# Optimization experiments

Hardware: AMD Instinct MI355X
Metric: run time of the kernel (lower is better)

Reference implementation:

```python
import jax, jax.numpy as jnp
import numpy as np
from jax import lax

DIM = 128
N_CODEBOOKS = 8
CODEBOOK_SIZE = 2048
BATCH = 16
TOKENS = 2048


def setup_inputs() -> dict:
    key = jax.random.key(0)
    k1, k2 = jax.random.split(key)
    x = jax.random.normal(k1, (BATCH, DIM, TOKENS), dtype=jnp.float32)
    # matches nn.Parameter(torch.randn(K, D) / D**0.5) per stage, stacked
    codebooks = jax.random.normal(k2, (N_CODEBOOKS, CODEBOOK_SIZE, DIM),
                                  dtype=jnp.float32) / jnp.sqrt(jnp.float32(DIM))
    return {"x": x, "codebooks": codebooks}


def reference(x, codebooks):
    """Residual VQ forward.

    x: (B, D, T), codebooks: (n_cb, K, D)
    Returns (total_quantized (B,D,T), codes (B,n_cb,T) int32, commitment_loss scalar)
    """
    xt = jnp.transpose(x, (0, 2, 1))  # (B, T, D)

    def step(carry, cb):
        residual, total = carry  # (B,T,D) each; cb: (K,D)
        # squared euclidean distances: ||r||^2 - 2 r.c + ||c||^2 -> (B,T,K)
        dist = (jnp.sum(residual * residual, axis=-1, keepdims=True)
                - 2.0 * jnp.einsum('btd,kd->btk', residual, cb)
                + jnp.sum(cb * cb, axis=-1))
        idx = jnp.argmin(dist, axis=-1)          # (B, T)
        quantized = cb[idx]                       # gather -> (B, T, D)
        # straight-through combine
        q_st = residual + lax.stop_gradient(quantized - residual)
        total = total + q_st
        residual = residual - lax.stop_gradient(quantized)
        # F.mse_loss(residual.detach(), zeros) == mean(residual**2), detached
        loss = jnp.mean(lax.stop_gradient(residual) ** 2)
        return (residual, total), (idx.astype(jnp.int32), loss)

    init = (xt, jnp.zeros_like(xt))
    (_, total), (codes, losses) = lax.scan(step, init, codebooks)
    total_quantized = jnp.transpose(total, (0, 2, 1))   # (B, D, T)
    codes = jnp.transpose(codes, (1, 0, 2))             # (B, n_cb, T)
    commitment_loss = jnp.sum(losses)
    return total_quantized, codes, commitment_loss
```

## Files before the change

kernel.cpp:

```cpp
#include <hip/hip_runtime.h>

#define DIM 128
#define NCB 8
#define KSZ 2048
#define BATCH 16
#define TOK 2048
#define NTOK (BATCH * TOK)
#define NELEM (BATCH * DIM * TOK)
#define T_TILE 128
#define NTHR 512
#define CHUNK 64
#define NCHUNK (KSZ / CHUNK)

typedef float f32x4 __attribute__((ext_vector_type(4)));
typedef short s16x8 __attribute__((ext_vector_type(8)));

__device__ __forceinline__ unsigned short f2bf(float f) {
    unsigned u = __float_as_uint(f);
    u = (u + 0x7FFFu + ((u >> 16) & 1u)) >> 16;
    return (unsigned short)u;
}
__device__ __forceinline__ float bf2f(unsigned short h) {
    return __uint_as_float(((unsigned)h) << 16);
}

__global__ void rvq_prep_hi(const float* __restrict__ cbs,
                            unsigned short* __restrict__ ch) {
    int i = blockIdx.x * 256 + threadIdx.x;
    ch[i] = f2bf(cbs[i]);
}

__global__ void rvq_cnorm(const float* __restrict__ cbs,
                          float* __restrict__ cnorm,
                          float* __restrict__ loss_acc) {
    if (blockIdx.x == 0 && threadIdx.x == 0) *loss_acc = 0.0f;
    int k = blockIdx.x * 256 + threadIdx.x;
    const float4* row = (const float4*)(cbs + (size_t)k * DIM);
    float s = 0.0f;
#pragma unroll
    for (int i = 0; i < DIM / 4; ++i) {
        float4 v = row[i];
        s += v.x * v.x + v.y * v.y + v.z * v.z + v.w * v.w;
    }
    cnorm[k] = s;
}

__global__ __launch_bounds__(NTHR, 2) void rvq_fused(
        const float* __restrict__ x,
        const float* __restrict__ cbs,
        const unsigned short* __restrict__ ch,
        const float* __restrict__ cng,
        float* __restrict__ out,
        float* __restrict__ codes,
        float* __restrict__ loss_acc) {
    __shared__ float res_lds[T_TILE][DIM + 4];
    __shared__ unsigned short Bbuf[2][8192];
    __shared__ float mv1[T_TILE * 16];
    __shared__ int   mi1[T_TILE * 16];
    __shared__ float mv2[T_TILE * 16];
    __shared__ int   mi2[T_TILE * 16];
    __shared__ int   best4s[T_TILE][4];

    const int tid   = threadIdx.x;
    const int lane  = tid & 63;
    const int wv    = __builtin_amdgcn_readfirstlane(tid >> 6);
    const int col16 = lane & 15;
    const int quad  = lane >> 4;

    const int token0 = blockIdx.x * T_TILE;
    const int b      = token0 >> 11;
    const int t_in_b = token0 & (TOK - 1);

    {
        const float* xb = x + (size_t)b * DIM * TOK + t_in_b;
#pragma unroll
        for (int it = 0; it < 8; ++it) {
            int idx = it * NTHR + tid;
            int d  = idx >> 5;
            int t4 = (idx & 31) * 4;
            float4 v = *(const float4*)(xb + (size_t)d * TOK + t4);
            res_lds[t4 + 0][d] = v.x;
            res_lds[t4 + 1][d] = v.y;
            res_lds[t4 + 2][d] = v.z;
            res_lds[t4 + 3][d] = v.w;
        }
    }
    __syncthreads();

    float my_loss = 0.0f;

#define STAGE_PREFETCH(cc)                                                     \
    {                                                                          \
        int _f0 = wv * 2, _f1 = wv * 2 + 1;                                    \
        stg0 = *(const s16x8*)(ch_s +                                          \
            ((size_t)((cc) * CHUNK + (_f0 >> 2) * 16 + col16)) * DIM +         \
            ((_f0 & 3) * 32 + quad * 8));                                      \
        stg1 = *(const s16x8*)(ch_s +                                          \
            ((size_t)((cc) * CHUNK + (_f1 >> 2) * 16 + col16)) * DIM +         \
            ((_f1 & 3) * 32 + quad * 8));                                      \
    }

#define STAGE_WRITE(buf)                                                       \
    {                                                                          \
        *(s16x8*)&Bbuf[buf][(wv * 2) * 512 + lane * 8]     = stg0;             \
        *(s16x8*)&Bbuf[buf][(wv * 2 + 1) * 512 + lane * 8] = stg1;             \
    }

#define COMPUTE(accv, buf)                                                     \
    {                                                                          \
        _Pragma("unroll")                                                      \
        for (int nt = 0; nt < 4; ++nt) accv[nt] = (f32x4){0.f, 0.f, 0.f, 0.f}; \
        _Pragma("unroll")                                                      \
        for (int dc = 0; dc < 4; ++dc) {                                       \
            s16x8 bh0 = *(const s16x8*)&Bbuf[buf][(0 + dc) * 512 + lane * 8];  \
            s16x8 bh1 = *(const s16x8*)&Bbuf[buf][(4 + dc) * 512 + lane * 8];  \
            s16x8 bh2 = *(const s16x8*)&Bbuf[buf][(8 + dc) * 512 + lane * 8];  \
            s16x8 bh3 = *(const s16x8*)&Bbuf[buf][(12 + dc) * 512 + lane * 8]; \
            accv[0] = __builtin_amdgcn_mfma_f32_16x16x32_bf16(ah[dc], bh0, accv[0], 0, 0, 0); \
            accv[1] = __builtin_amdgcn_mfma_f32_16x16x32_bf16(ah[dc], bh1, accv[1], 0, 0, 0); \
            accv[2] = __builtin_amdgcn_mfma_f32_16x16x32_bf16(ah[dc], bh2, accv[2], 0, 0, 0); \
            accv[3] = __builtin_amdgcn_mfma_f32_16x16x32_bf16(ah[dc], bh3, accv[3], 0, 0, 0); \
            accv[0] = __builtin_amdgcn_mfma_f32_16x16x32_bf16(al[dc], bh0, accv[0], 0, 0, 0); \
            accv[1] = __builtin_amdgcn_mfma_f32_16x16x32_bf16(al[dc], bh1, accv[1], 0, 0, 0); \
            accv[2] = __builtin_amdgcn_mfma_f32_16x16x32_bf16(al[dc], bh2, accv[2], 0, 0, 0); \
            accv[3] = __builtin_amdgcn_mfma_f32_16x16x32_bf16(al[dc], bh3, accv[3], 0, 0, 0); \
        }                                                                      \
    }

#define FOLD(accv, cc)                                                         \
    {                                                                          \
        int _ib0 = (cc) * CHUNK + col16;                                       \
        float _cn0 = cn_s[_ib0], _cn1 = cn_s[_ib0 + 16];                       \
        float _cn2 = cn_s[_ib0 + 32], _cn3 = cn_s[_ib0 + 48];                  \
        _Pragma("unroll")                                                      \
        for (int r = 0; r < 4; ++r) {                                          \
            float p0 = fmaf(-2.0f, accv[0][r], _cn0);                          \
            float p1 = fmaf(-2.0f, accv[1][r], _cn1);                          \
            float p2 = fmaf(-2.0f, accv[2][r], _cn2);                          \
            float p3 = fmaf(-2.0f, accv[3][r], _cn3);                          \
            bool c01 = p1 < p0;                                                \
            float m01 = c01 ? p1 : p0; int j01 = c01 ? _ib0 + 16 : _ib0;       \
            bool c23 = p3 < p2;                                                \
            float m23 = c23 ? p3 : p2; int j23 = c23 ? _ib0 + 48 : _ib0 + 32;  \
            bool cf = m23 < m01;                                               \
            float m = cf ? m23 : m01; int jm = cf ? j23 : j01;                 \
            bool b1 = m < v1[r];                                               \
            bool b2 = m < v2[r];                                               \
            v2[r] = b1 ? v1[r] : (b2 ? m : v2[r]);                             \
            i2[r] = b1 ? i1[r] : (b2 ? jm : i2[r]);                            \
            v1[r] = b1 ? m : v1[r];                                            \
            i1[r] = b1 ? jm : i1[r];                                           \
        }                                                                      \
    }

#pragma unroll 1
    for (int s = 0; s < NCB; ++s) {
        const unsigned short* __restrict__ ch_s = ch  + (size_t)s * KSZ * DIM;
        const float* __restrict__ cb_s = cbs + (size_t)s * KSZ * DIM;
        const float* __restrict__ cn_s = cng + (size_t)s * KSZ;

        s16x8 ah[4], al[4];
#pragma unroll
        for (int dc = 0; dc < 4; ++dc) {
            int t  = wv * 16 + col16;
            int d0 = dc * 32 + quad * 8;
            float4 u = *(const float4*)&res_lds[t][d0];
            float4 w = *(const float4*)&res_lds[t][d0 + 4];
            float e[8] = {u.x, u.y, u.z, u.w, w.x, w.y, w.z, w.w};
            s16x8 hv, lv;
#pragma unroll
            for (int j = 0; j < 8; ++j) {
                unsigned short h = f2bf(e[j]);
                hv[j] = (short)h;
                lv[j] = (short)f2bf(e[j] - bf2f(h));
            }
            ah[dc] = hv;
            al[dc] = lv;
        }

        float v1[4], v2[4]; int i1[4], i2[4];
#pragma unroll
        for (int r = 0; r < 4; ++r) {
            v1[r] = 3.4e38f; v2[r] = 3.4e38f; i1[r] = 0; i2[r] = 0;
        }

        s16x8 stg0, stg1;
        f32x4 accA[4], accB[4];

        STAGE_PREFETCH(0); STAGE_WRITE(0); __syncthreads();
        STAGE_PREFETCH(1);
        COMPUTE(accA, 0);
        STAGE_WRITE(1); __syncthreads();
#pragma unroll 1
        for (int c = 1; c < 31; c += 2) {
            STAGE_PREFETCH(c + 1);
            COMPUTE(accB, 1);
            FOLD(accA, c - 1);
            STAGE_WRITE(0);
            __syncthreads();
            STAGE_PREFETCH(c + 2);
            COMPUTE(accA, 0);
            FOLD(accB, c);
            STAGE_WRITE(1);
            __syncthreads();
        }
        COMPUTE(accB, 1);
        FOLD(accA, 30);
        FOLD(accB, 31);

#pragma unroll
        for (int r = 0; r < 4; ++r) {
            int t = wv * 16 + quad * 4 + r;
            mv1[t * 16 + col16] = v1[r];
            mi1[t * 16 + col16] = i1[r];
            mv2[t * 16 + col16] = v2[r];
            mi2[t * 16 + col16] = i2[r];
        }
        __syncthreads();

        if (tid < T_TILE) {
            const int t = tid;
            float bv[4] = {3.4e38f, 3.4e38f, 3.4e38f, 3.4e38f};
            int   bi[4] = {0x7FFFFFFF, 0x7FFFFFFF, 0x7FFFFFFF, 0x7FFFFFFF};
#pragma unroll
            for (int col = 0; col < 16; ++col) {
#pragma unroll
                for (int w = 0; w < 2; ++w) {
                    float v = w ? mv2[t * 16 + col] : mv1[t * 16 + col];
                    int   i = w ? mi2[t * 16 + col] : mi1[t * 16 + col];
#pragma unroll
                    for (int j = 0; j < 4; ++j) {
                        if (v < bv[j] || (v == bv[j] && i < bi[j])) {
                            float tv = bv[j]; bv[j] = v; v = tv;
                            int   ti = bi[j]; bi[j] = i; i = ti;
                        }
                    }
                }
            }
#pragma unroll
            for (int j = 0; j < 4; ++j) best4s[t][j] = bi[j];
        }
        __syncthreads();

        {
            const int t  = tid >> 2;
            const int cs = tid & 3;
            const int cand = best4s[t][cs];
            const float* crow = cb_s + (size_t)cand * DIM;
            float n0 = 0, n1 = 0, n2 = 0, n3 = 0;
            float a0 = 0, a1 = 0, a2 = 0, a3 = 0;
#pragma unroll 8
            for (int d4 = 0; d4 < DIM / 4; ++d4) {
                float4 r4 = *(const float4*)&res_lds[t][d4 * 4];
                float4 q4 = *(const float4*)&crow[d4 * 4];
                n0 = fmaf(r4.x, r4.x, n0); n1 = fmaf(r4.y, r4.y, n1);
                n2 = fmaf(r4.z, r4.z, n2); n3 = fmaf(r4.w, r4.w, n3);
                a0 = fmaf(r4.x, q4.x, a0); a1 = fmaf(r4.y, q4.y, a1);
                a2 = fmaf(r4.z, q4.z, a2); a3 = fmaf(r4.w, q4.w, a3);
            }
            float rn  = (n0 + n1) + (n2 + n3);
            float dot = (a0 + a1) + (a2 + a3);
            float dist = fmaf(-2.0f, dot, rn) + cn_s[cand];
            int best = cand;
#pragma unroll
            for (int mk = 1; mk <= 2; mk <<= 1) {
                float od = __shfl_xor(dist, mk, 64);
                int   oi = __shfl_xor(best, mk, 64);
                if (od < dist || (od == dist && oi < best)) {
                    dist = od; best = oi;
                }
            }
            if (cs == 0)
                codes[(size_t)b * (NCB * TOK) + (size_t)s * TOK + t_in_b + t] =
                    (float)best;
            const float* qrow = cb_s + (size_t)best * DIM;
            float lp = 0.0f;
#pragma unroll
            for (int d4 = 0; d4 < 8; ++d4) {
                int d = cs * 32 + d4 * 4;
                float4 r4 = *(const float4*)&res_lds[t][d];
                float4 q4 = *(const float4*)&qrow[d];
                float4 nr;
                nr.x = r4.x - q4.x; nr.y = r4.y - q4.y;
                nr.z = r4.z - q4.z; nr.w = r4.w - q4.w;
                *(float4*)&res_lds[t][d] = nr;
                lp += nr.x * nr.x + nr.y * nr.y + nr.z * nr.z + nr.w * nr.w;
            }
            my_loss += lp;
        }
        __syncthreads();
    }

    {
        const float* xb = x + (size_t)b * DIM * TOK + t_in_b;
        float* ob = out + (size_t)b * DIM * TOK + t_in_b;
#pragma unroll
        for (int it = 0; it < 8; ++it) {
            int idx = it * NTHR + tid;
            int d  = idx >> 5;
            int t4 = (idx & 31) * 4;
            float4 v = *(const float4*)(xb + (size_t)d * TOK + t4);
            float4 o;
            o.x = v.x - res_lds[t4 + 0][d];
            o.y = v.y - res_lds[t4 + 1][d];
            o.z = v.z - res_lds[t4 + 2][d];
            o.w = v.w - res_lds[t4 + 3][d];
            *(float4*)(ob + (size_t)d * TOK + t4) = o;
        }
    }

#pragma unroll
    for (int off = 32; off > 0; off >>= 1)
        my_loss += __shfl_down(my_loss, off, 64);
    if (lane == 0) atomicAdd(loss_acc, my_loss);
}

__global__ void rvq_loss_fin(const float* __restrict__ loss_acc,
                             float* __restrict__ loss_out) {
    *loss_out = *loss_acc * (1.0f / (float)NELEM);
}

extern "C" void kernel_launch(void* const* d_in, const int* in_sizes, int n_in,
                              void* d_out, int out_size, void* d_ws, size_t ws_size,
                              hipStream_t stream) {
    const float* x   = (const float*)d_in[0];
    const float* cbs = (const float*)d_in[1];

    float* out      = (float*)d_out;
    float* codes    = out + NELEM;
    float* loss_out = out + NELEM + (size_t)BATCH * NCB * TOK;

    float* wsf      = (float*)d_ws;
    float* loss_acc = wsf;
    unsigned short* ch = (unsigned short*)(wsf + 256);
    float* cng = (float*)(ch + (size_t)NCB * KSZ * DIM);

    hipLaunchKernelGGL(rvq_prep_hi, dim3((NCB * KSZ * DIM) / 256), dim3(256),
                       0, stream, cbs, ch);
    hipLaunchKernelGGL(rvq_cnorm, dim3((NCB * KSZ) / 256), dim3(256), 0, stream,
                       cbs, cng, loss_acc);
    hipLaunchKernelGGL(rvq_fused, dim3(NTOK / T_TILE), dim3(NTHR), 0, stream,
                       x, cbs, ch, cng, out, codes, loss_acc);
    hipLaunchKernelGGL(rvq_loss_fin, dim3(1), dim3(1), 0, stream,
                       loss_acc, loss_out);
}
```

Measured before the change: 548.6 us.

## Switch RVQ distance GEMM to single-pass fp16 MFMA with grouped top-2 candidates

Drops the bf16 hi/lo split, which needed two MFMA passes, in favour of a single fp16 MFMA pass, halving the matrix work per codebook. Work is reorganised so each pair of waves owns a 512-code group and covers 64 tokens × 32 codes per chunk, reusing A fragments across four M-tiles. Chunk IDs are packed into the low mantissa bits so the running top-2 is kept with plain fminf/fmaxf instead of index tracking. Per-group top-2 values then feed an exact fp32 rescoring of four candidates per group. This risks wrong argmin choices from the fp16 rounding and the mantissa-bit packing, and raises register pressure from the 16-slot state and ah[4][4].

Result: slower. 603.6 us (+10.0%).

```diff
diff --git a/kernel.cpp b/kernel.cpp
--- a/kernel.cpp
+++ b/kernel.cpp
@@ -9,25 +9,17 @@
 #define NELEM (BATCH * DIM * TOK)
 #define T_TILE 128
 #define NTHR 512
-#define CHUNK 64
-#define NCHUNK (KSZ / CHUNK)
+#define CHUNK 32
+#define NCHUNK 16
+#define GCODES 512
 
 typedef float f32x4 __attribute__((ext_vector_type(4)));
-typedef short s16x8 __attribute__((ext_vector_type(8)));
-
-__device__ __forceinline__ unsigned short f2bf(float f) {
-    unsigned u = __float_as_uint(f);
-    u = (u + 0x7FFFu + ((u >> 16) & 1u)) >> 16;
-    return (unsigned short)u;
-}
-__device__ __forceinline__ float bf2f(unsigned short h) {
-    return __uint_as_float(((unsigned)h) << 16);
-}
-
-__global__ void rvq_prep_hi(const float* __restrict__ cbs,
-                            unsigned short* __restrict__ ch) {
+typedef _Float16 f16x8 __attribute__((ext_vector_type(8)));
+
+__global__ void rvq_prep_f16(const float* __restrict__ cbs,
+                             _Float16* __restrict__ chf) {
     int i = blockIdx.x * 256 + threadIdx.x;
-    ch[i] = f2bf(cbs[i]);
+    chf[i] = (_Float16)cbs[i];
 }
 
 __global__ void rvq_cnorm(const float* __restrict__ cbs,
@@ -48,24 +40,25 @@
 __global__ __launch_bounds__(NTHR, 2) void rvq_fused(
         const float* __restrict__ x,
         const float* __restrict__ cbs,
-        const unsigned short* __restrict__ ch,
+        const _Float16* __restrict__ chf,
         const float* __restrict__ cng,
         float* __restrict__ out,
         float* __restrict__ codes,
         float* __restrict__ loss_acc) {
     __shared__ float res_lds[T_TILE][DIM + 4];
-    __shared__ unsigned short Bbuf[2][8192];
-    __shared__ float mv1[T_TILE * 16];
-    __shared__ int   mi1[T_TILE * 16];
-    __shared__ float mv2[T_TILE * 16];
-    __shared__ int   mi2[T_TILE * 16];
-    __shared__ int   best4s[T_TILE][4];
+    __shared__ __align__(16) char shbuf[T_TILE * 144 * 4];
+    __shared__ float cn_lds[KSZ];
+
+    _Float16* Ball = (_Float16*)shbuf;
+    float*    cand = (float*)shbuf;
 
     const int tid   = threadIdx.x;
     const int lane  = tid & 63;
     const int wv    = __builtin_amdgcn_readfirstlane(tid >> 6);
     const int col16 = lane & 15;
     const int quad  = lane >> 4;
+    const int g     = wv >> 1;
+    const int sub   = wv & 1;
 
     const int token0 = blockIdx.x * T_TILE;
     const int b      = token0 >> 11;
@@ -88,198 +81,228 @@
     __syncthreads();
 
     float my_loss = 0.0f;
-
-#define STAGE_PREFETCH(cc)                                                     \
-    {                                                                          \
-        int _f0 = wv * 2, _f1 = wv * 2 + 1;                                    \
-        stg0 = *(const s16x8*)(ch_s +                                          \
-            ((size_t)((cc) * CHUNK + (_f0 >> 2) * 16 + col16)) * DIM +         \
-            ((_f0 & 3) * 32 + quad * 8));                                      \
-        stg1 = *(const s16x8*)(ch_s +                                          \
-            ((size_t)((cc) * CHUNK + (_f1 >> 2) * 16 + col16)) * DIM +         \
-            ((_f1 & 3) * 32 + quad * 8));                                      \
-    }
-
-#define STAGE_WRITE(buf)                                                       \
-    {                                                                          \
-        *(s16x8*)&Bbuf[buf][(wv * 2) * 512 + lane * 8]     = stg0;             \
-        *(s16x8*)&Bbuf[buf][(wv * 2 + 1) * 512 + lane * 8] = stg1;             \
-    }
-
-#define COMPUTE(accv, buf)                                                     \
-    {                                                                          \
-        _Pragma("unroll")                                                      \
-        for (int nt = 0; nt < 4; ++nt) accv[nt] = (f32x4){0.f, 0.f, 0.f, 0.f}; \
-        _Pragma("unroll")                                                      \
-        for (int dc = 0; dc < 4; ++dc) {                                       \
-            s16x8 bh0 = *(const s16x8*)&Bbuf[buf][(0 + dc) * 512 + lane * 8];  \
-            s16x8 bh1 = *(const s16x8*)&Bbuf[buf][(4 + dc) * 512 + lane * 8];  \
-            s16x8 bh2 = *(const s16x8*)&Bbuf[buf][(8 + dc) * 512 + lane * 8];  \
-            s16x8 bh3 = *(const s16x8*)&Bbuf[buf][(12 + dc) * 512 + lane * 8]; \
-            accv[0] = __builtin_amdgcn_mfma_f32_16x16x32_bf16(ah[dc], bh0, accv[0], 0, 0, 0); \
-            accv[1] = __builtin_amdgcn_mfma_f32_16x16x32_bf16(ah[dc], bh1, accv[1], 0, 0, 0); \
-            accv[2] = __builtin_amdgcn_mfma_f32_16x16x32_bf16(ah[dc], bh2, accv[2], 0, 0, 0); \
-            accv[3] = __builtin_amdgcn_mfma_f32_16x16x32_bf16(ah[dc], bh3, accv[3], 0, 0, 0); \
-            accv[0] = __builtin_amdgcn_mfma_f32_16x16x32_bf16(al[dc], bh0, accv[0], 0, 0, 0); \
-            accv[1] = __builtin_amdgcn_mfma_f32_16x16x32_bf16(al[dc], bh1, accv[1], 0, 0, 0); \
-            accv[2] = __builtin_amdgcn_mfma_f32_16x16x32_bf16(al[dc], bh2, accv[2], 0, 0, 0); \
-            accv[3] = __builtin_amdgcn_mfma_f32_16x16x32_bf16(al[dc], bh3, accv[3], 0, 0, 0); \
-        }                                                                      \
-    }
-
-#define FOLD(accv, cc)                                                         \
-    {                                                                          \
-        int _ib0 = (cc) * CHUNK + col16;                                       \
-        float _cn0 = cn_s[_ib0], _cn1 = cn_s[_ib0 + 16];                       \
-        float _cn2 = cn_s[_ib0 + 32], _cn3 = cn_s[_ib0 + 48];                  \
-        _Pragma("unroll")                                                      \
-        for (int r = 0; r < 4; ++r) {                                          \
-            float p0 = fmaf(-2.0f, accv[0][r], _cn0);                          \
-            float p1 = fmaf(-2.0f, accv[1][r], _cn1);                          \
-            float p2 = fmaf(-2.0f, accv[2][r], _cn2);                          \
-            float p3 = fmaf(-2.0f, accv[3][r], _cn3);                          \
-            bool c01 = p1 < p0;                                                \
-            float m01 = c01 ? p1 : p0; int j01 = c01 ? _ib0 + 16 : _ib0;       \
-            bool c23 = p3 < p2;                                                \
-            float m23 = c23 ? p3 : p2; int j23 = c23 ? _ib0 + 48 : _ib0 + 32;  \
-            bool cf = m23 < m01;                                               \
-            float m = cf ? m23 : m01; int jm = cf ? j23 : j01;                 \
-            bool b1 = m < v1[r];                                               \
-            bool b2 = m < v2[r];                                               \
-            v2[r] = b1 ? v1[r] : (b2 ? m : v2[r]);                             \
-            i2[r] = b1 ? i1[r] : (b2 ? jm : i2[r]);                            \
-            v1[r] = b1 ? m : v1[r];                                            \
-            i1[r] = b1 ? jm : i1[r];                                           \
-        }                                                                      \
-    }
+    const float INFV = __builtin_inff();
 
 #pragma unroll 1
     for (int s = 0; s < NCB; ++s) {
-        const unsigned short* __restrict__ ch_s = ch  + (size_t)s * KSZ * DIM;
+        const _Float16* __restrict__ ch_s = chf + (size_t)s * KSZ * DIM;
         const float* __restrict__ cb_s = cbs + (size_t)s * KSZ * DIM;
         const float* __restrict__ cn_s = cng + (size_t)s * KSZ;
 
-        s16x8 ah[4], al[4];
-#pragma unroll
-        for (int dc = 0; dc < 4; ++dc) {
-            int t  = wv * 16 + col16;
-            int d0 = dc * 32 + quad * 8;
-            float4 u = *(const float4*)&res_lds[t][d0];
-            float4 w = *(const float4*)&res_lds[t][d0 + 4];
-            float e[8] = {u.x, u.y, u.z, u.w, w.x, w.y, w.z, w.w};
-            s16x8 hv, lv;
-#pragma unroll
-            for (int j = 0; j < 8; ++j) {
-                unsigned short h = f2bf(e[j]);
-                hv[j] = (short)h;
-                lv[j] = (short)f2bf(e[j] - bf2f(h));
-            }
-            ah[dc] = hv;
-            al[dc] = lv;
-        }
-
-        float v1[4], v2[4]; int i1[4], i2[4];
-#pragma unroll
-        for (int r = 0; r < 4; ++r) {
-            v1[r] = 3.4e38f; v2[r] = 3.4e38f; i1[r] = 0; i2[r] = 0;
-        }
-
-        s16x8 stg0, stg1;
-        f32x4 accA[4], accB[4];
-
-        STAGE_PREFETCH(0); STAGE_WRITE(0); __syncthreads();
-        STAGE_PREFETCH(1);
-        COMPUTE(accA, 0);
-        STAGE_WRITE(1); __syncthreads();
+        {
+            float4 v = *(const float4*)(cn_s + tid * 4);
+            *(float4*)&cn_lds[tid * 4] = v;
+        }
+
+        f16x8 ah[4][4];
+#pragma unroll
+        for (int mt = 0; mt < 4; ++mt) {
+#pragma unroll
+            for (int dc = 0; dc < 4; ++dc) {
+                int t  = sub * 64 + mt * 16 + col16;
+                int d0 = dc * 32 + quad * 8;
+                float4 u = *(const float4*)&res_lds[t][d0];
+                float4 w = *(const float4*)&res_lds[t][d0 + 4];
+                f16x8 hv;
+                hv[0] = (_Float16)u.x; hv[1] = (_Float16)u.y;
+                hv[2] = (_Float16)u.z; hv[3] = (_Float16)u.w;
+                hv[4] = (_Float16)w.x; hv[5] = (_Float16)w.y;
+                hv[6] = (_Float16)w.z; hv[7] = (_Float16)w.w;
+                ah[mt][dc] = hv;
+            }
+        }
+
+        float k1[16], k2[16];
+#pragma unroll
+        for (int sl = 0; sl < 16; ++sl) { k1[sl] = INFV; k2[sl] = INFV; }
+
+        f16x8 stg[4];
+        _Float16* Bg = Ball + g * 2 * 4096;
+
+#pragma unroll
+        for (int j = 0; j < 4; ++j) {
+            int f = sub * 4 + j;
+            int nt = f >> 2, dc = f & 3;
+            stg[j] = *(const f16x8*)(ch_s +
+                (size_t)(g * GCODES + nt * 16 + col16) * DIM + dc * 32 + quad * 8);
+        }
+#pragma unroll
+        for (int j = 0; j < 4; ++j) {
+            int f = sub * 4 + j;
+            *(f16x8*)(Bg + f * 512 + lane * 8) = stg[j];
+        }
+        __syncthreads();
+
+        f32x4 acc[4][2];
 #pragma unroll 1
-        for (int c = 1; c < 31; c += 2) {
-            STAGE_PREFETCH(c + 1);
-            COMPUTE(accB, 1);
-            FOLD(accA, c - 1);
-            STAGE_WRITE(0);
+        for (int c = 0; c < NCHUNK; ++c) {
+            const int cur = c & 1;
+            if (c < NCHUNK - 1) {
+#pragma unroll
+                for (int j = 0; j < 4; ++j) {
+                    int f = sub * 4 + j;
+                    int nt = f >> 2, dc = f & 3;
+                    stg[j] = *(const f16x8*)(ch_s +
+                        (size_t)(g * GCODES + (c + 1) * CHUNK + nt * 16 + col16) * DIM
+                        + dc * 32 + quad * 8);
+                }
+            }
+#pragma unroll
+            for (int mt = 0; mt < 4; ++mt) {
+                acc[mt][0] = (f32x4){0.f, 0.f, 0.f, 0.f};
+                acc[mt][1] = (f32x4){0.f, 0.f, 0.f, 0.f};
+            }
+#pragma unroll
+            for (int dc = 0; dc < 4; ++dc) {
+                f16x8 b0 = *(const f16x8*)(Bg + cur * 4096 + dc * 512 + lane * 8);
+                f16x8 b1 = *(const f16x8*)(Bg + cur * 4096 + (4 + dc) * 512 + lane * 8);
+#pragma unroll
+                for (int mt = 0; mt < 4; ++mt) {
+                    acc[mt][0] = __builtin_amdgcn_mfma_f32_16x16x32_f16(
+                        ah[mt][dc], b0, acc[mt][0], 0, 0, 0);
+                    acc[mt][1] = __builtin_amdgcn_mfma_f32_16x16x32_f16(
+                        ah[mt][dc], b1, acc[mt][1], 0, 0, 0);
+                }
+            }
+            {
+                float cn0 = cn_lds[g * GCODES + c * CHUNK + col16];
+                float cn1 = cn_lds[g * GCODES + c * CHUNK + 16 + col16];
+                unsigned em = (unsigned)(c << 1);
+#pragma unroll
+                for (int mt = 0; mt < 4; ++mt) {
+#pragma unroll
+                    for (int r = 0; r < 4; ++r) {
+                        float p0 = fmaf(-2.0f, acc[mt][0][r], cn0);
+                        float p1 = fmaf(-2.0f, acc[mt][1][r], cn1);
+                        float q0 = __uint_as_float(
+                            (__float_as_uint(p0) & 0xFFFFFFE0u) | em);
+                        float q1 = __uint_as_float(
+                            (__float_as_uint(p1) & 0xFFFFFFE0u) | em | 1u);
+                        float m = fminf(q0, q1);
+                        int sl = mt * 4 + r;
+                        k2[sl] = fminf(k2[sl], fmaxf(k1[sl], m));
+                        k1[sl] = fminf(k1[sl], m);
+                    }
+                }
+            }
+            if (c < NCHUNK - 1) {
+#pragma unroll
+                for (int j = 0; j < 4; ++j) {
+                    int f = sub * 4 + j;
+                    *(f16x8*)(Bg + (cur ^ 1) * 4096 + f * 512 + lane * 8) = stg[j];
+                }
+            }
             __syncthreads();
-            STAGE_PREFETCH(c + 2);
-            COMPUTE(accA, 0);
-            FOLD(accB, c);
-            STAGE_WRITE(1);
-            __syncthreads();
-        }
-        COMPUTE(accB, 1);
-        FOLD(accA, 30);
-        FOLD(accB, 31);
-
-#pragma unroll
-        for (int r = 0; r < 4; ++r) {
-            int t = wv * 16 + quad * 4 + r;
-            mv1[t * 16 + col16] = v1[r];
-            mi1[t * 16 + col16] = i1[r];
-            mv2[t * 16 + col16] = v2[r];
-            mi2[t * 16 + col16] = i2[r];
-        }
-        __syncthreads();
-
-        if (tid < T_TILE) {
-            const int t = tid;
-            float bv[4] = {3.4e38f, 3.4e38f, 3.4e38f, 3.4e38f};
-            int   bi[4] = {0x7FFFFFFF, 0x7FFFFFFF, 0x7FFFFFFF, 0x7FFFFFFF};
-#pragma unroll
-            for (int col = 0; col < 16; ++col) {
-#pragma unroll
-                for (int w = 0; w < 2; ++w) {
-                    float v = w ? mv2[t * 16 + col] : mv1[t * 16 + col];
-                    int   i = w ? mi2[t * 16 + col] : mi1[t * 16 + col];
-#pragma unroll
-                    for (int j = 0; j < 4; ++j) {
-                        if (v < bv[j] || (v == bv[j] && i < bi[j])) {
-                            float tv = bv[j]; bv[j] = v; v = tv;
-                            int   ti = bi[j]; bi[j] = i; i = ti;
-                        }
-                    }
-                }
-            }
-#pragma unroll
-            for (int j = 0; j < 4; ++j) best4s[t][j] = bi[j];
+        }
+
+#pragma unroll
+        for (int mt = 0; mt < 4; ++mt) {
+#pragma unroll
+            for (int r = 0; r < 4; ++r) {
+                int t = sub * 64 + mt * 16 + quad * 4 + r;
+                int sl = mt * 4 + r;
+                float2 pr; pr.x = k1[sl]; pr.y = k2[sl];
+                *(float2*)&cand[t * 144 + g * 36 + col16 * 2] = pr;
+            }
         }
         __syncthreads();
 
         {
             const int t  = tid >> 2;
-            const int cs = tid & 3;
-            const int cand = best4s[t][cs];
-            const float* crow = cb_s + (size_t)cand * DIM;
+            const int gg = tid & 3;
+            float bk[4];
+            int   bcol[4];
+#pragma unroll
+            for (int jj = 0; jj < 4; ++jj) { bk[jj] = INFV; bcol[jj] = 0; }
+            const float* base = &cand[t * 144 + gg * 36];
+#pragma unroll
+            for (int j = 0; j < 8; ++j) {
+                float4 v4 = *(const float4*)(base + j * 4);
+                float vv[4] = {v4.x, v4.y, v4.z, v4.w};
+#pragma unroll
+                for (int e = 0; e < 4; ++e) {
+                    float v = vv[e];
+                    int col = (j * 4 + e) >> 1;
+#pragma unroll
+                    for (int jj = 0; jj < 4; ++jj) {
+                        bool lt = v < bk[jj];
+                        float tv = bk[jj]; int tc = bcol[jj];
+                        bk[jj] = lt ? v : bk[jj];
+                        bcol[jj] = lt ? col : bcol[jj];
+                        v = lt ? tv : v;
+                        col = lt ? tc : col;
+                    }
+                }
+            }
+            int cds[4];
+#pragma unroll
+            for (int jj = 0; jj < 4; ++jj) {
+                unsigned e = __float_as_uint(bk[jj]) & 0x1Fu;
+                cds[jj] = gg * GCODES + (int)((e >> 1) << 5) +
+                          (int)((e & 1) << 4) + bcol[jj];
+            }
+            const float* p0 = cb_s + (size_t)cds[0] * DIM;
+            const float* p1 = cb_s + (size_t)cds[1] * DIM;
+            const float* p2 = cb_s + (size_t)cds[2] * DIM;
+            const float* p3 = cb_s + (size_t)cds[3] * DIM;
             float n0 = 0, n1 = 0, n2 = 0, n3 = 0;
-            float a0 = 0, a1 = 0, a2 = 0, a3 = 0;
+            float a[4][4];
+#pragma unroll
+            for (int jj = 0; jj < 4; ++jj)
+#pragma unroll
+                for (int e = 0; e < 4; ++e) a[jj][e] = 0.0f;
 #pragma unroll 8
             for (int d4 = 0; d4 < DIM / 4; ++d4) {
                 float4 r4 = *(const float4*)&res_lds[t][d4 * 4];
-                float4 q4 = *(const float4*)&crow[d4 * 4];
                 n0 = fmaf(r4.x, r4.x, n0); n1 = fmaf(r4.y, r4.y, n1);
                 n2 = fmaf(r4.z, r4.z, n2); n3 = fmaf(r4.w, r4.w, n3);
-                a0 = fmaf(r4.x, q4.x, a0); a1 = fmaf(r4.y, q4.y, a1);
-                a2 = fmaf(r4.z, q4.z, a2); a3 = fmaf(r4.w, q4.w, a3);
-            }
-            float rn  = (n0 + n1) + (n2 + n3);
-            float dot = (a0 + a1) + (a2 + a3);
-            float dist = fmaf(-2.0f, dot, rn) + cn_s[cand];
-            int best = cand;
+                float4 q0 = *(const float4*)(p0 + d4 * 4);
+                a[0][0] = fmaf(r4.x, q0.x, a[0][0]);
+                a[0][1] = fmaf(r4.y, q0.y, a[0][1]);
+                a[0][2] = fmaf(r4.z, q0.z, a[0][2]);
+                a[0][3] = fmaf(r4.w, q0.w, a[0][3]);
+                float4 q1 = *(const float4*)(p1 + d4 * 4);
+                a[1][0] = fmaf(r4.x, q1.x, a[1][0]);
+                a[1][1] = fmaf(r4.y, q1.y, a[1][1]);
+                a[1][2] = fmaf(r4.z, q1.z, a[1][2]);
+                a[1][3] = fmaf(r4.w, q1.w, a[1][3]);
+                float4 q2 = *(const float4*)(p2 + d4 * 4);
+                a[2][0] = fmaf(r4.x, q2.x, a[2][0]);
+                a[2][1] = fmaf(r4.y, q2.y, a[2][1]);
+                a[2][2] = fmaf(r4.z, q2.z, a[2][2]);
+                a[2][3] = fmaf(r4.w, q2.w, a[2][3]);
+                float4 q3 = *(const float4*)(p3 + d4 * 4);
+                a[3][0] = fmaf(r4.x, q3.x, a[3][0]);
+                a[3][1] = fmaf(r4.y, q3.y, a[3][1]);
+                a[3][2] = fmaf(r4.z, q3.z, a[3][2]);
+                a[3][3] = fmaf(r4.w, q3.w, a[3][3]);
+            }
+            float rn = (n0 + n1) + (n2 + n3);
+            float bd = INFV; int bc = 0x7FFFFFFF;
+#pragma unroll
+            for (int jj = 0; jj < 4; ++jj) {
+                float dot = (a[jj][0] + a[jj][1]) + (a[jj][2] + a[jj][3]);
+                float dist = fmaf(-2.0f, dot, rn) + cn_s[cds[jj]];
+                if (dist < bd || (dist == bd && cds[jj] < bc)) {
+                    bd = dist; bc = cds[jj];
+                }
+            }
 #pragma unroll
             for (int mk = 1; mk <= 2; mk <<= 1) {
-                float od = __shfl_xor(dist, mk, 64);
-                int   oi = __shfl_xor(best, mk, 64);
-                if (od < dist || (od == dist && oi < best)) {
-                    dist = od; best = oi;
-                }
-            }
-            if (cs == 0)
+                float od = __shfl_xor(bd, mk, 64);
+                int   oc = __shfl_xor(bc, mk, 64);
+                if (od < bd || (od == bd && oc < bc)) { bd = od; bc = oc; }
+            }
+            if (gg == 0)
                 codes[(size_t)b * (NCB * TOK) + (size_t)s * TOK + t_in_b + t] =
-                    (float)best;
-            const float* qrow = cb_s + (size_t)best * DIM;
+                    (float)bc;
+            const float* qrow = cb_s + (size_t)bc * DIM;
             float lp = 0.0f;
 #pragma unroll
             for (int d4 = 0; d4 < 8; ++d4) {
-                int d = cs * 32 + d4 * 4;
+                int d = gg * 32 + d4 * 4;
                 float4 r4 = *(const float4*)&res_lds[t][d];
-                float4 q4 = *(const float4*)&qrow[d];
+                float4 q4 = *(const float4*)(qrow + d);
                 float4 nr;
                 nr.x = r4.x - q4.x; nr.y = r4.y - q4.y;
                 nr.z = r4.z - q4.z; nr.w = r4.w - q4.w;
@@ -332,15 +355,15 @@
 
     float* wsf      = (float*)d_ws;
     float* loss_acc = wsf;
-    unsigned short* ch = (unsigned short*)(wsf + 256);
-    float* cng = (float*)(ch + (size_t)NCB * KSZ * DIM);
-
-    hipLaunchKernelGGL(rvq_prep_hi, dim3((NCB * KSZ * DIM) / 256), dim3(256),
-                       0, stream, cbs, ch);
+    _Float16* chf   = (_Float16*)(wsf + 256);
+    float* cng      = (float*)(chf + (size_t)NCB * KSZ * DIM);
+
+    hipLaunchKernelGGL(rvq_prep_f16, dim3((NCB * KSZ * DIM) / 256), dim3(256),
+                       0, stream, cbs, chf);
     hipLaunchKernelGGL(rvq_cnorm, dim3((NCB * KSZ) / 256), dim3(256), 0, stream,
                        cbs, cng, loss_acc);
     hipLaunchKernelGGL(rvq_fused, dim3(NTOK / T_TILE), dim3(NTHR), 0, stream,
-                       x, cbs, ch, cng, out, codes, loss_acc);
+                       x, cbs, chf, cng, out, codes, loss_acc);
     hipLaunchKernelGGL(rvq_loss_fin, dim3(1), dim3(1), 0, stream,
                        loss_acc, loss_out);
 }
```
